# Kernel tuning notes

Measured on AMD Instinct MI355X. Metric: run time of the kernel, lower is better.

Reference implementation:

```python
import jax, jax.numpy as jnp
import numpy as np

B, T, H = 16, 512, 512

def _gru_layer(x, h0, wih, whh, bih, bhh, reverse):
    # x: [B,T,in], h0: [B,H]; PyTorch gate order r,z,n in the 3H axis.
    xg = jnp.einsum('bti,gi->btg', x, wih) + bih  # [B,T,3H] input-side gates, precomputed
    def step(h, xg_t):
        gh = h @ whh.T + bhh  # [B,3H]
        xr, xz, xn = jnp.split(xg_t, 3, axis=-1)
        hr, hz, hn = jnp.split(gh, 3, axis=-1)
        r = jax.nn.sigmoid(xr + hr)
        z = jax.nn.sigmoid(xz + hz)
        n = jnp.tanh(xn + r * hn)
        h_new = (1.0 - z) * n + z * h
        return h_new, h_new
    _, ys = jax.lax.scan(step, h0, jnp.swapaxes(xg, 0, 1), reverse=reverse)  # [T,B,H]
    return jnp.swapaxes(ys, 0, 1)

def _forward(x, h1, h2,
             wih_l0f, whh_l0f, bih_l0f, bhh_l0f, wih_l0b, whh_l0b, bih_l0b, bhh_l0b,
             wih_l1f, whh_l1f, bih_l1f, bhh_l1f, wih_l1b, whh_l1b, bih_l1b, bhh_l1b,
             wih_l2f, whh_l2f, bih_l2f, bhh_l2f, wih_l2b, whh_l2b, bih_l2b, bhh_l2b,
             g2_wih, g2_whh, g2_bih, g2_bhh, fc_w, fc_b):
    layers = [((wih_l0f, whh_l0f, bih_l0f, bhh_l0f), (wih_l0b, whh_l0b, bih_l0b, bhh_l0b)),
              ((wih_l1f, whh_l1f, bih_l1f, bhh_l1f), (wih_l1b, whh_l1b, bih_l1b, bhh_l1b)),
              ((wih_l2f, whh_l2f, bih_l2f, bhh_l2f), (wih_l2b, whh_l2b, bih_l2b, bhh_l2b))]
    out = x
    for l, (pf, pb) in enumerate(layers):
        of = _gru_layer(out, h1[2 * l], *pf, reverse=False)
        ob = _gru_layer(out, h1[2 * l + 1], *pb, reverse=True)
        out = jnp.concatenate([of, ob], axis=-1)  # [B,T,2H]
    out2 = _gru_layer(out, h2[0], g2_wih, g2_whh, g2_bih, g2_bhh, reverse=False)  # [B,T,H]
    logits = out2[:, -1, :] @ fc_w.T + fc_b  # [B,1]
    return (jax.nn.sigmoid(logits), out2)

def setup_inputs():
    key = jax.random.key(0)
    ks = jax.random.split(key, 40)
    cnt = iter(range(40))
    s = jnp.float32(0.04)
    d = {}
    d['x'] = jax.random.normal(ks[next(cnt)], (B, T, 2048), jnp.float32)
    d['h1'] = jax.random.normal(ks[next(cnt)], (6, B, H), jnp.float32) * s
    d['h2'] = jax.random.normal(ks[next(cnt)], (1, B, H), jnp.float32) * s
    in_dims = [2048, 2 * H, 2 * H]
    for l in range(3):
        for dr in 'fb':
            d[f'wih_l{l}{dr}'] = jax.random.normal(ks[next(cnt)], (3 * H, in_dims[l]), jnp.float32) * s
            d[f'whh_l{l}{dr}'] = jax.random.normal(ks[next(cnt)], (3 * H, H), jnp.float32) * s
            d[f'bih_l{l}{dr}'] = jax.random.normal(ks[next(cnt)], (3 * H,), jnp.float32) * s
            d[f'bhh_l{l}{dr}'] = jax.random.normal(ks[next(cnt)], (3 * H,), jnp.float32) * s
    d['g2_wih'] = jax.random.normal(ks[next(cnt)], (3 * H, 2 * H), jnp.float32) * s
    d['g2_whh'] = jax.random.normal(ks[next(cnt)], (3 * H, H), jnp.float32) * s
    d['g2_bih'] = jax.random.normal(ks[next(cnt)], (3 * H,), jnp.float32) * s
    d['g2_bhh'] = jax.random.normal(ks[next(cnt)], (3 * H,), jnp.float32) * s
    d['fc_w'] = jax.random.normal(ks[next(cnt)], (1, H), jnp.float32) * s
    d['fc_b'] = jax.random.normal(ks[next(cnt)], (1,), jnp.float32) * s
    return d

def reference(x, h1, h2,
              wih_l0f, whh_l0f, bih_l0f, bhh_l0f, wih_l0b, whh_l0b, bih_l0b, bhh_l0b,
              wih_l1f, whh_l1f, bih_l1f, bhh_l1f, wih_l1b, whh_l1b, bih_l1b, bhh_l1b,
              wih_l2f, whh_l2f, bih_l2f, bhh_l2f, wih_l2b, whh_l2b, bih_l2b, bhh_l2b,
              g2_wih, g2_whh, g2_bih, g2_bhh, fc_w, fc_b):
    return _forward(x, h1, h2,
                    wih_l0f, whh_l0f, bih_l0f, bhh_l0f, wih_l0b, whh_l0b, bih_l0b, bhh_l0b,
                    wih_l1f, whh_l1f, bih_l1f, bhh_l1f, wih_l1b, whh_l1b, bih_l1b, bhh_l1b,
                    wih_l2f, whh_l2f, bih_l2f, bhh_l2f, wih_l2b, whh_l2b, bih_l2b, bhh_l2b,
                    g2_wih, g2_whh, g2_bih, g2_bhh, fc_w, fc_b)
```

## Files before the change

### kernel.cpp

```cpp
#include <hip/hip_runtime.h>
#include <cstdint>
#include <cstddef>

typedef unsigned short u16;
typedef unsigned int u32;
typedef __attribute__((ext_vector_type(8))) short bf16x8;
typedef __attribute__((ext_vector_type(4))) float f32x4;

#define T_SEQ 512
#define HID 512

__device__ __forceinline__ u16 f2bf(float f) {
  union { float f; u32 i; } c; c.f = f;
  u32 r = (c.i + 0x7FFFu + ((c.i >> 16) & 1u)) >> 16;
  return (u16)r;
}
__device__ __forceinline__ u16 f2h(float f) {
  union { _Float16 h; u16 u; } c; c.h = (_Float16)f; return c.u;
}
__device__ __forceinline__ float h2f(u16 u) {
  union { u16 u; _Float16 h; } c; c.u = u; return (float)c.h;
}
__device__ __forceinline__ float sigmf(float x) { return 1.f / (1.f + __expf(-x)); }
__device__ __forceinline__ float tanhfast(float x) {
  float e = __expf(2.f * x); return 1.f - 2.f / (e + 1.f);
}

template <int AF32>
__launch_bounds__(256)
__global__ void gemm_xg(const void* __restrict__ Av,
                        const float* __restrict__ W0, const float* __restrict__ W1,
                        const float* __restrict__ b0, const float* __restrict__ b1,
                        u16* __restrict__ xg0, u16* __restrict__ xg1, int K) {
  const int dir = blockIdx.z;
  const float* W = dir ? W1 : W0;
  const float* bias = dir ? b1 : b0;
  u16* xg = dir ? xg1 : xg0;
  const int bm = blockIdx.x, bn = blockIdx.y;
  const int tid = threadIdx.x, lane = tid & 63, wv = tid >> 6;
  const int wm = wv & 1, wn = wv >> 1, quad = lane >> 4, l15 = lane & 15;

  __shared__ u16 As[128 * 40];
  __shared__ u16 Bs[128 * 40];

  f32x4 acc[4][4] = {};
  const float* Wb = W + (size_t)(bn * 128) * K;

  for (int k0 = 0; k0 < K; k0 += 32) {
    __syncthreads();
    if constexpr (AF32) {
      const float* Ab = (const float*)Av + (size_t)(bm * 128) * K;
#pragma unroll
      for (int it = 0; it < 4; ++it) {
        int c = tid + it * 256;
        int row = c >> 3, kp = (c & 7) * 4;
        float4 v = *(const float4*)(Ab + (size_t)row * K + k0 + kp);
        ushort4 s = { f2bf(v.x), f2bf(v.y), f2bf(v.z), f2bf(v.w) };
        *(ushort4*)(&As[row * 40 + kp]) = s;
      }
    } else {
      const u16* Ab = (const u16*)Av + (size_t)(bm * 128) * K;
#pragma unroll
      for (int it = 0; it < 2; ++it) {
        int c = tid + it * 256;
        int row = c >> 2, kp = (c & 3) * 8;
        *(bf16x8*)(&As[row * 40 + kp]) = *(const bf16x8*)(Ab + (size_t)row * K + k0 + kp);
      }
    }
#pragma unroll
    for (int it = 0; it < 4; ++it) {
      int c = tid + it * 256;
      int row = c >> 3, kp = (c & 7) * 4;
      float4 v = *(const float4*)(Wb + (size_t)row * K + k0 + kp);
      ushort4 s = { f2bf(v.x), f2bf(v.y), f2bf(v.z), f2bf(v.w) };
      *(ushort4*)(&Bs[row * 40 + kp]) = s;
    }
    __syncthreads();
    bf16x8 af[4], bf[4];
#pragma unroll
    for (int i = 0; i < 4; ++i) {
      af[i] = *(const bf16x8*)(&As[(wm * 64 + i * 16 + l15) * 40 + quad * 8]);
      bf[i] = *(const bf16x8*)(&Bs[(wn * 64 + i * 16 + l15) * 40 + quad * 8]);
    }
#pragma unroll
    for (int mi = 0; mi < 4; ++mi)
#pragma unroll
      for (int ni = 0; ni < 4; ++ni)
        acc[mi][ni] = __builtin_amdgcn_mfma_f32_16x16x32_bf16(af[mi], bf[ni], acc[mi][ni], 0, 0, 0);
  }

#pragma unroll
  for (int ni = 0; ni < 4; ++ni) {
    int n = bn * 128 + wn * 64 + ni * 16 + l15;
    float bv = bias[n];
#pragma unroll
    for (int mi = 0; mi < 4; ++mi) {
      int m0 = bm * 128 + wm * 64 + mi * 16 + quad * 4;
#pragma unroll
      for (int r = 0; r < 4; ++r)
        xg[(size_t)(m0 + r) * 1536 + n] = f2h(acc[mi][ni][r] + bv);
    }
  }
}

__launch_bounds__(256, 1)
__global__ void gru_rec(const u16* __restrict__ xg_f, const u16* __restrict__ xg_b,
                        const float* __restrict__ whh_f, const float* __restrict__ whh_b,
                        const float* __restrict__ bhh_f, const float* __restrict__ bhh_b,
                        const float* __restrict__ h0_f, const float* __restrict__ h0_b,
                        void* __restrict__ outp, int out_stride, int out_f32,
                        u16* __restrict__ hbuf, int* __restrict__ flags_base, int Tn) {
  const int dir = blockIdx.y;
  const u16* xg    = dir ? xg_b  : xg_f;
  const float* whh = dir ? whh_b : whh_f;
  const float* bhh = dir ? bhh_b : bhh_f;
  const float* h0  = dir ? h0_b  : h0_f;
  const int w = blockIdx.x;
  const int tid = threadIdx.x, lane = tid & 63, q = tid >> 6;
  const int quad = lane >> 4, l15 = lane & 15;
  const int j = w * 64 + q * 16 + l15;
  const int myflag = w * 4 + q;
  int* flags = flags_base + dir * 64;
  u16* hb0 = hbuf + (dir * 2 + 0) * (16 * 512);
  u16* hb1 = hbuf + (dir * 2 + 1) * (16 * 512);
  const int dir_off = dir * 512;

  bf16x8 wfr[3][16];
#pragma unroll
  for (int g = 0; g < 3; ++g) {
    const float* wp = whh + (size_t)(g * 512 + j) * 512 + quad * 8;
#pragma unroll
    for (int kt = 0; kt < 16; ++kt) {
      float4 a = *(const float4*)(wp + kt * 32);
      float4 b = *(const float4*)(wp + kt * 32 + 4);
      bf16x8 fr;
      fr[0] = (short)f2bf(a.x); fr[1] = (short)f2bf(a.y);
      fr[2] = (short)f2bf(a.z); fr[3] = (short)f2bf(a.w);
      fr[4] = (short)f2bf(b.x); fr[5] = (short)f2bf(b.y);
      fr[6] = (short)f2bf(b.z); fr[7] = (short)f2bf(b.w);
      wfr[g][kt] = fr;
    }
  }
  float bh[3];
#pragma unroll
  for (int g = 0; g < 3; ++g) bh[g] = bhh[g * 512 + j];

  float hp4[4];
  u32 sv[4];
#pragma unroll
  for (int r = 0; r < 4; ++r) {
    int b = quad * 4 + r;
    hp4[r] = h0[b * 512 + j];
    u32 m = f2bf(hp4[r]);
    u32 nb = (u32)__shfl_xor((int)m, 1);
    sv[r] = m | (nb << 16);
  }
  if (!(l15 & 1)) {
#pragma unroll
    for (int r = 0; r < 4; ++r)
      __hip_atomic_store((u32*)(hb1 + (quad * 4 + r) * 512 + j), sv[r],
                         __ATOMIC_RELAXED, __HIP_MEMORY_SCOPE_AGENT);
  }
  if (lane == 0)
    __hip_atomic_store(&flags[myflag], 1, __ATOMIC_RELEASE, __HIP_MEMORY_SCOPE_AGENT);

  for (int t = 0; t < Tn; ++t) {
    const int te = dir ? (Tn - 1 - t) : t;
    u16 xgv[3][4];
#pragma unroll
    for (int g = 0; g < 3; ++g)
#pragma unroll
      for (int r = 0; r < 4; ++r)
        xgv[g][r] = xg[(size_t)((quad * 4 + r) * Tn + te) * 1536 + g * 512 + j];

    const int need = t + 1;
    int fv = __hip_atomic_load(&flags[lane & 31], __ATOMIC_ACQUIRE, __HIP_MEMORY_SCOPE_AGENT);
    while (__any(fv < need)) {
      __builtin_amdgcn_s_sleep(1);
      fv = __hip_atomic_load(&flags[lane & 31], __ATOMIC_ACQUIRE, __HIP_MEMORY_SCOPE_AGENT);
    }

    const u16* hsrc = (t & 1) ? hb0 : hb1;
    const u16* hp = hsrc + l15 * 512 + quad * 8;
    bf16x8 afr[16];
#pragma unroll
    for (int kt = 0; kt < 16; ++kt) afr[kt] = *(const bf16x8*)(hp + kt * 32);

    f32x4 acc[3] = {};
#pragma unroll
    for (int kt = 0; kt < 16; ++kt)
#pragma unroll
      for (int g = 0; g < 3; ++g)
        acc[g] = __builtin_amdgcn_mfma_f32_16x16x32_bf16(afr[kt], wfr[g][kt], acc[g], 0, 0, 0);

    u16* hbw = (t & 1) ? hb1 : hb0;
    float hv4[4];
#pragma unroll
    for (int r = 0; r < 4; ++r) {
      float xr = h2f(xgv[0][r]);
      float xz = h2f(xgv[1][r]);
      float xn = h2f(xgv[2][r]);
      float rg = sigmf(xr + acc[0][r] + bh[0]);
      float zg = sigmf(xz + acc[1][r] + bh[1]);
      float ng = tanhfast(xn + rg * (acc[2][r] + bh[2]));
      float hv = (1.f - zg) * ng + zg * hp4[r];
      hp4[r] = hv;
      hv4[r] = hv;
      u32 m = f2bf(hv);
      u32 nb = (u32)__shfl_xor((int)m, 1);
      sv[r] = m | (nb << 16);
    }
    if (!(l15 & 1)) {
#pragma unroll
      for (int r = 0; r < 4; ++r)
        __hip_atomic_store((u32*)(hbw + (quad * 4 + r) * 512 + j), sv[r],
                           __ATOMIC_RELAXED, __HIP_MEMORY_SCOPE_AGENT);
    }
    if (lane == 0)
      __hip_atomic_store(&flags[myflag], t + 2, __ATOMIC_RELEASE, __HIP_MEMORY_SCOPE_AGENT);

    if (out_f32) {
#pragma unroll
      for (int r = 0; r < 4; ++r)
        ((float*)outp)[(size_t)((quad * 4 + r) * Tn + te) * out_stride + dir_off + j] = hv4[r];
    } else if (!(l15 & 1)) {
#pragma unroll
      for (int r = 0; r < 4; ++r)
        *(u32*)((u16*)outp + (size_t)((quad * 4 + r) * Tn + te) * out_stride + dir_off + j) = sv[r];
    }
  }
}

__global__ void fc_kernel(const float* __restrict__ out2, const float* __restrict__ fc_w,
                          const float* __restrict__ fc_b, float* __restrict__ dst) {
  int b = blockIdx.x, lane = threadIdx.x;
  const float* row = out2 + ((size_t)b * T_SEQ + (T_SEQ - 1)) * HID;
  float s = 0.f;
  for (int jj = lane; jj < HID; jj += 64) s += row[jj] * fc_w[jj];
#pragma unroll
  for (int off = 32; off > 0; off >>= 1) s += __shfl_down(s, off, 64);
  if (lane == 0) dst[b] = sigmf(s + fc_b[0]);
}

extern "C" void kernel_launch(void* const* d_in, const int* in_sizes, int n_in,
                              void* d_out, int out_size, void* d_ws, size_t ws_size,
                              hipStream_t stream) {
  const float* x  = (const float*)d_in[0];
  const float* h1 = (const float*)d_in[1];
  const float* h2 = (const float*)d_in[2];
  auto P = [&](int i) { return (const float*)d_in[i]; };

  u16* xg0 = (u16*)d_ws;
  u16* xg1 = xg0 + (size_t)8192 * 1536;
  u16* outb = xg1 + (size_t)8192 * 1536;
  u16* hbuf = outb + (size_t)8192 * 1024;
  int* flags = (int*)(hbuf + 4 * 8192);
  float* out_f = (float*)d_out;
  float* out2 = out_f + 16;

  hipMemsetAsync(flags, 0, 4 * 128 * sizeof(int), stream);

  gemm_xg<1><<<dim3(64, 12, 2), 256, 0, stream>>>(x, P(3), P(7), P(5), P(9), xg0, xg1, 2048);
  gru_rec<<<dim3(8, 2), 256, 0, stream>>>(xg0, xg1, P(4), P(8), P(6), P(10),
                                          h1, h1 + 8192, outb, 1024, 0, hbuf, flags, T_SEQ);
  gemm_xg<0><<<dim3(64, 12, 2), 256, 0, stream>>>(outb, P(11), P(15), P(13), P(17), xg0, xg1, 1024);
  gru_rec<<<dim3(8, 2), 256, 0, stream>>>(xg0, xg1, P(12), P(16), P(14), P(18),
                                          h1 + 2 * 8192, h1 + 3 * 8192, outb, 1024, 0, hbuf,
                                          flags + 128, T_SEQ);
  gemm_xg<0><<<dim3(64, 12, 2), 256, 0, stream>>>(outb, P(19), P(23), P(21), P(25), xg0, xg1, 1024);
  gru_rec<<<dim3(8, 2), 256, 0, stream>>>(xg0, xg1, P(20), P(24), P(22), P(26),
                                          h1 + 4 * 8192, h1 + 5 * 8192, outb, 1024, 0, hbuf,
                                          flags + 256, T_SEQ);
  gemm_xg<0><<<dim3(64, 12, 1), 256, 0, stream>>>(outb, P(27), P(27), P(29), P(29), xg0, xg1, 1024);
  gru_rec<<<dim3(8, 1), 256, 0, stream>>>(xg0, xg0, P(28), P(28), P(30), P(30),
                                          h2, h2, out2, 512, 1, hbuf, flags + 384, T_SEQ);
  fc_kernel<<<16, 64, 0, stream>>>(out2, P(31), P(32), out_f);
}
```

Before: 14.55 ms.

## Prefetch next-step input gates and relax flag polling to atomic loads

Moves the load of the next timestep's precomputed input gates to after the flag publish, so it overlaps the wait for other blocks instead of sitting on the critical path. The flag poll switches from acquire to relaxed loads, and the hidden-state reads become relaxed 64-bit atomic loads, which avoids the cache invalidation that acquire semantics imply on each poll. Output stores become nontemporal. The risk is memory ordering: correctness now depends on the relaxed atomic reads observing data published with the release store, which HIP does not strictly guarantee without an acquire.

```diff
diff --git a/kernel.cpp b/kernel.cpp
--- a/kernel.cpp
+++ b/kernel.cpp
@@ -4,6 +4,7 @@
 
 typedef unsigned short u16;
 typedef unsigned int u32;
+typedef unsigned long long u64;
 typedef __attribute__((ext_vector_type(8))) short bf16x8;
 typedef __attribute__((ext_vector_type(4))) float f32x4;
 
@@ -164,27 +165,37 @@
   if (lane == 0)
     __hip_atomic_store(&flags[myflag], 1, __ATOMIC_RELEASE, __HIP_MEMORY_SCOPE_AGENT);
 
+  u16 xgv[3][4];
+  {
+    const int te0 = dir ? (Tn - 1) : 0;
+#pragma unroll
+    for (int g = 0; g < 3; ++g)
+#pragma unroll
+      for (int r = 0; r < 4; ++r)
+        xgv[g][r] = xg[(size_t)((quad * 4 + r) * Tn + te0) * 1536 + g * 512 + j];
+  }
+
   for (int t = 0; t < Tn; ++t) {
     const int te = dir ? (Tn - 1 - t) : t;
-    u16 xgv[3][4];
-#pragma unroll
-    for (int g = 0; g < 3; ++g)
-#pragma unroll
-      for (int r = 0; r < 4; ++r)
-        xgv[g][r] = xg[(size_t)((quad * 4 + r) * Tn + te) * 1536 + g * 512 + j];
-
     const int need = t + 1;
-    int fv = __hip_atomic_load(&flags[lane & 31], __ATOMIC_ACQUIRE, __HIP_MEMORY_SCOPE_AGENT);
+    int fv = __hip_atomic_load(&flags[lane & 31], __ATOMIC_RELAXED, __HIP_MEMORY_SCOPE_AGENT);
     while (__any(fv < need)) {
       __builtin_amdgcn_s_sleep(1);
-      fv = __hip_atomic_load(&flags[lane & 31], __ATOMIC_ACQUIRE, __HIP_MEMORY_SCOPE_AGENT);
+      fv = __hip_atomic_load(&flags[lane & 31], __ATOMIC_RELAXED, __HIP_MEMORY_SCOPE_AGENT);
     }
 
     const u16* hsrc = (t & 1) ? hb0 : hb1;
     const u16* hp = hsrc + l15 * 512 + quad * 8;
     bf16x8 afr[16];
 #pragma unroll
-    for (int kt = 0; kt < 16; ++kt) afr[kt] = *(const bf16x8*)(hp + kt * 32);
+    for (int kt = 0; kt < 16; ++kt) {
+      union { u64 qq[2]; bf16x8 v; } u;
+      u.qq[0] = __hip_atomic_load((const u64*)(hp + kt * 32),
+                                  __ATOMIC_RELAXED, __HIP_MEMORY_SCOPE_AGENT);
+      u.qq[1] = __hip_atomic_load((const u64*)(hp + kt * 32 + 4),
+                                  __ATOMIC_RELAXED, __HIP_MEMORY_SCOPE_AGENT);
+      afr[kt] = u.v;
+    }
 
     f32x4 acc[3] = {};
 #pragma unroll
@@ -193,7 +204,6 @@
       for (int g = 0; g < 3; ++g)
         acc[g] = __builtin_amdgcn_mfma_f32_16x16x32_bf16(afr[kt], wfr[g][kt], acc[g], 0, 0, 0);
 
-    u16* hbw = (t & 1) ? hb1 : hb0;
     float hv4[4];
 #pragma unroll
     for (int r = 0; r < 4; ++r) {
@@ -210,6 +220,7 @@
       u32 nb = (u32)__shfl_xor((int)m, 1);
       sv[r] = m | (nb << 16);
     }
+    u16* hbw = (t & 1) ? hb1 : hb0;
     if (!(l15 & 1)) {
 #pragma unroll
       for (int r = 0; r < 4; ++r)
@@ -219,14 +230,25 @@
     if (lane == 0)
       __hip_atomic_store(&flags[myflag], t + 2, __ATOMIC_RELEASE, __HIP_MEMORY_SCOPE_AGENT);
 
+    if (t + 1 < Tn) {
+      const int tn = dir ? (Tn - 2 - t) : (t + 1);
+#pragma unroll
+      for (int g = 0; g < 3; ++g)
+#pragma unroll
+        for (int r = 0; r < 4; ++r)
+          xgv[g][r] = xg[(size_t)((quad * 4 + r) * Tn + tn) * 1536 + g * 512 + j];
+    }
+
     if (out_f32) {
 #pragma unroll
       for (int r = 0; r < 4; ++r)
-        ((float*)outp)[(size_t)((quad * 4 + r) * Tn + te) * out_stride + dir_off + j] = hv4[r];
+        __builtin_nontemporal_store(
+            hv4[r], (float*)outp + (size_t)((quad * 4 + r) * Tn + te) * out_stride + dir_off + j);
     } else if (!(l15 & 1)) {
 #pragma unroll
       for (int r = 0; r < 4; ++r)
-        *(u32*)((u16*)outp + (size_t)((quad * 4 + r) * Tn + te) * out_stride + dir_off + j) = sv[r];
+        __builtin_nontemporal_store(
+            sv[r], (u32*)((u16*)outp + (size_t)((quad * 4 + r) * Tn + te) * out_stride + dir_off + j));
     }
   }
 }
```

Result: slower. 15.91 ms (+9.4%).
